# Kernel tuning notes

Hardware: AMD Instinct MI355X
Metric: run time of the kernel (lower is better)

The kernel has to match this reference:

```python
import jax, jax.numpy as jnp
import numpy as np

B, DIN, DH, DOUT = 4096, 512, 1024, 256
DFF = 4 * DH
STEPS = 30
REF_DIM = 64
GAMMA = 0.5 * min(1.0, float(np.sqrt(REF_DIM / DIN)))  # dimension-scaled gamma
LN_EPS = 1e-5


def setup_inputs() -> dict:
    key = jax.random.key(0)
    ks = jax.random.split(key, 6)
    rn = lambda k, shp, s: (jax.random.normal(k, shp, jnp.float32) * s)
    return {
        "x": rn(ks[0], (B, DIN), 1.0),
        "embed_w": rn(ks[1], (DH, DIN), 0.02),
        "embed_b": jnp.zeros((DH,), jnp.float32),
        "W1": rn(ks[2], (DFF, DH), 0.02),
        "b1": jnp.zeros((DFF,), jnp.float32),
        "W2": rn(ks[3], (DH, DFF), 0.02),
        "b2": jnp.zeros((DH,), jnp.float32),
        "ln_g": jnp.ones((DH,), jnp.float32),
        "ln_b": jnp.zeros((DH,), jnp.float32),
        "head_w": rn(ks[4], (DOUT, DH), 0.02),
        "head_b": jnp.zeros((DOUT,), jnp.float32),
    }


def _spectral_normalize(W, n_iter=15):
    # power iteration (u, v treated as constants, like torch spectral_norm buffers)
    v0 = jnp.full((W.shape[1],), 1.0 / np.sqrt(W.shape[1]), W.dtype)
    def body(i, uv):
        _, v = uv
        u = W @ v
        u = u / (jnp.linalg.norm(u) + 1e-12)
        v = W.T @ u
        v = v / (jnp.linalg.norm(v) + 1e-12)
        return (u, v)
    u0 = W @ v0
    u0 = u0 / (jnp.linalg.norm(u0) + 1e-12)
    u, v = jax.lax.fori_loop(0, n_iter, body, (u0, v0))
    u = jax.lax.stop_gradient(u)
    v = jax.lax.stop_gradient(v)
    sigma = u @ (W @ v)  # grad flows through W here, as in torch
    return W / sigma


def _layernorm(h, g, b):
    mu = jnp.mean(h, axis=-1, keepdims=True)
    var = jnp.var(h, axis=-1, keepdims=True)
    return (h - mu) * jax.lax.rsqrt(var + LN_EPS) * g + b


def reference(x, embed_w, embed_b, W1, b1, W2, b2, ln_g, ln_b, head_w, head_b):
    W1n = _spectral_normalize(W1)
    W2n = _spectral_normalize(W2)
    x_emb = x @ embed_w.T + embed_b  # [B, DH]; constant across steps

    def ffn(h):
        hn = _layernorm(h, ln_g, ln_b)
        hid = jnp.tanh(hn @ W1n.T + b1)  # dropout p=0 -> identity
        return hid @ W2n.T + b2

    def step(h, _):
        h_target = ffn(h) + x_emb
        h_next = (1.0 - GAMMA) * h + GAMMA * h_target
        return h_next, None

    h, _ = jax.lax.scan(step, x_emb, None, length=STEPS)
    return h @ head_w.T + head_b
```

## Files before the change

### kernel.cpp

```cpp
#include <hip/hip_runtime.h>
#include <hip/hip_bf16.h>
#include <math.h>

#define B_    4096
#define DIN_  512
#define DH_   1024
#define DOUT_ 256
#define DFF_  4096
#define STEPS_ 30
#define GAMMA_ 0.17677669529663687f
#define LN_EPS_ 1e-5f

typedef __attribute__((ext_vector_type(8))) short short8;
typedef __attribute__((ext_vector_type(4))) float f32x4;

__device__ inline void gload_lds16(const void* g, void* l) {
  __builtin_amdgcn_global_load_lds(
      (const __attribute__((address_space(1))) unsigned int*)g,
      (__attribute__((address_space(3))) unsigned int*)l, 16, 0, 0);
}

__device__ inline float fast_tanh(float v) {
  const float e = __expf(2.f * v);
  return 1.f - 2.f * __builtin_amdgcn_rcpf(e + 1.f);
}

__device__ inline float bf2f(unsigned short u) {
  return __uint_as_float((unsigned)u << 16);
}

__global__ __launch_bounds__(512, 2) void gemm256(
    const __hip_bfloat16* __restrict__ A, const __hip_bfloat16* __restrict__ Bm,
    int M, int N, int K, int kc, int nt, const float* __restrict__ bias,
    int epi, __hip_bfloat16* __restrict__ bf16out) {
  __shared__ __align__(16) char lds[131072];
  const int tid = threadIdx.x;
  const int lane = tid & 63;
  const int wid = tid >> 6;
  const int wr = wid >> 2;
  const int wc = wid & 3;

  const int gx = gridDim.x;
  const int nwg = gx * gridDim.y;
  const int wg = blockIdx.y * gx + blockIdx.x;
  const int cpx = nwg >> 3;
  const int swz = (wg & 7) * cpx + (wg >> 3);
  const int bx = swz % gx, by = swz / gx;
  const int m0 = by * 256, n0 = bx * 256;
  const int zk = blockIdx.z * kc;

  const int scol = ((lane & 7) ^ (lane >> 3)) * 8;
  const int srow = lane >> 3;

  f32x4 acc[8][4];
  const f32x4 zero = {0.f, 0.f, 0.f, 0.f};
#pragma unroll
  for (int i = 0; i < 8; ++i)
#pragma unroll
    for (int j = 0; j < 4; ++j) acc[i][j] = zero;

  auto STAGE = [&](int t) {
    const int kt = zk + t * 64;
    char* ab = &lds[(t & 1) * 32768];
    char* bb = &lds[65536 + (t & 1) * 32768];
#pragma unroll
    for (int i = 0; i < 4; ++i) {
      const int rbase = wid * 32 + i * 8;
      const int r = rbase + srow;
      gload_lds16(A + (size_t)(m0 + r) * K + kt + scol, ab + rbase * 128);
      gload_lds16(Bm + (size_t)(n0 + r) * K + kt + scol, bb + rbase * 128);
    }
  };

  STAGE(0);
  STAGE(1);

  const int ar = lane & 15;
  const int hi = lane >> 4;
  const int a7 = ar & 7;
  const int co0 = ((0 * 4 + hi) ^ a7) * 16;
  const int co1 = ((1 * 4 + hi) ^ a7) * 16;

  for (int t = 0; t < nt; ++t) {
    const int buf = t & 1;
    const char* Ab = &lds[buf * 32768];
    const char* Bb = &lds[65536 + buf * 32768];
    const int arow = (wr * 128 + ar) * 128;
    const int brow = (wc * 64 + ar) * 128;

    if (t == nt - 1) {
      asm volatile("s_waitcnt vmcnt(0)" ::: "memory");
    } else {
      asm volatile("s_waitcnt vmcnt(8)" ::: "memory");
    }
    __builtin_amdgcn_s_barrier();
    __builtin_amdgcn_sched_barrier(0);

    short8 a[4][2], b[4][2];
#pragma unroll
    for (int i = 0; i < 4; ++i) {
      a[i][0] = *(const short8*)(Ab + arow + i * 2048 + co0);
      a[i][1] = *(const short8*)(Ab + arow + i * 2048 + co1);
    }
#pragma unroll
    for (int j = 0; j < 2; ++j) {
      b[j][0] = *(const short8*)(Bb + brow + j * 2048 + co0);
      b[j][1] = *(const short8*)(Bb + brow + j * 2048 + co1);
    }
    asm volatile("s_waitcnt lgkmcnt(0)" ::: "memory");
    __builtin_amdgcn_sched_barrier(0);
    __builtin_amdgcn_s_setprio(1);
#pragma unroll
    for (int i = 0; i < 4; ++i)
#pragma unroll
      for (int j = 0; j < 2; ++j)
#pragma unroll
        for (int ks = 0; ks < 2; ++ks)
          acc[i][j] = __builtin_amdgcn_mfma_f32_16x16x32_bf16(a[i][ks], b[j][ks], acc[i][j], 0, 0, 0);
    __builtin_amdgcn_s_setprio(0);
    __builtin_amdgcn_sched_barrier(0);
#pragma unroll
    for (int j = 0; j < 2; ++j) {
      b[2 + j][0] = *(const short8*)(Bb + brow + (2 + j) * 2048 + co0);
      b[2 + j][1] = *(const short8*)(Bb + brow + (2 + j) * 2048 + co1);
    }
    asm volatile("s_waitcnt lgkmcnt(0)" ::: "memory");
    __builtin_amdgcn_sched_barrier(0);
    __builtin_amdgcn_s_setprio(1);
#pragma unroll
    for (int i = 0; i < 4; ++i)
#pragma unroll
      for (int j = 0; j < 2; ++j)
#pragma unroll
        for (int ks = 0; ks < 2; ++ks)
          acc[i][2 + j] = __builtin_amdgcn_mfma_f32_16x16x32_bf16(a[i][ks], b[2 + j][ks], acc[i][2 + j], 0, 0, 0);
    __builtin_amdgcn_s_setprio(0);
    __builtin_amdgcn_sched_barrier(0);
#pragma unroll
    for (int i = 0; i < 4; ++i) {
      a[i][0] = *(const short8*)(Ab + arow + (4 + i) * 2048 + co0);
      a[i][1] = *(const short8*)(Ab + arow + (4 + i) * 2048 + co1);
    }
    asm volatile("s_waitcnt lgkmcnt(0)" ::: "memory");
    __builtin_amdgcn_sched_barrier(0);
    __builtin_amdgcn_s_setprio(1);
#pragma unroll
    for (int i = 0; i < 4; ++i)
#pragma unroll
      for (int j = 0; j < 2; ++j)
#pragma unroll
        for (int ks = 0; ks < 2; ++ks)
          acc[4 + i][2 + j] = __builtin_amdgcn_mfma_f32_16x16x32_bf16(a[i][ks], b[2 + j][ks], acc[4 + i][2 + j], 0, 0, 0);
    __builtin_amdgcn_s_setprio(0);
    __builtin_amdgcn_sched_barrier(0);
    __builtin_amdgcn_s_setprio(1);
#pragma unroll
    for (int i = 0; i < 4; ++i)
#pragma unroll
      for (int j = 0; j < 2; ++j)
#pragma unroll
        for (int ks = 0; ks < 2; ++ks)
          acc[4 + i][j] = __builtin_amdgcn_mfma_f32_16x16x32_bf16(a[i][ks], b[j][ks], acc[4 + i][j], 0, 0, 0);
    __builtin_amdgcn_s_setprio(0);
    __builtin_amdgcn_sched_barrier(0);
    __builtin_amdgcn_s_barrier();
    __builtin_amdgcn_sched_barrier(0);
    if (t + 2 < nt) STAGE(t + 2);
  }

  if (epi == 4) bf16out += (size_t)blockIdx.z * ((size_t)M * N);
  const int rb = hi * 4;
#pragma unroll
  for (int mf = 0; mf < 8; ++mf) {
#pragma unroll
    for (int nf = 0; nf < 4; ++nf) {
      const int col = n0 + wc * 64 + nf * 16 + ar;
      const float bvs = bias ? bias[col] : 0.f;
#pragma unroll
      for (int j = 0; j < 4; ++j) {
        const int row = m0 + wr * 128 + mf * 16 + rb + j;
        float v = acc[mf][nf][j] + bvs;
        if (epi == 1) v = fast_tanh(v);
        bf16out[(size_t)row * N + col] = __float2bfloat16(v);
      }
    }
  }
}

__global__ __launch_bounds__(256) void gemm_bt(
    const __hip_bfloat16* __restrict__ A, const __hip_bfloat16* __restrict__ Bm,
    int M, int N, int K, const float* __restrict__ bias, int epi,
    float* __restrict__ f32out, float* __restrict__ f32out2) {
  __shared__ __align__(16) short As[128 * 32];
  __shared__ __align__(16) short Bs[128 * 32];
  const int tid = threadIdx.x;
  const int lane = tid & 63;
  const int wid = tid >> 6;
  const int wr = wid >> 1, wc = wid & 1;

  const int gx = gridDim.x;
  const int nwg = gx * gridDim.y;
  const int wg = blockIdx.y * gx + blockIdx.x;
  const int cpx = nwg >> 3;
  const int swz = (wg & 7) * cpx + (wg >> 3);
  const int bx = swz % gx, by = swz / gx;

  const int m0 = by * 128, n0 = bx * 128;
  const int ldsrow = lane >> 2;
  const int col8 = (lane & 3) * 8;

  f32x4 acc[4][4];
  const f32x4 zero = {0.f, 0.f, 0.f, 0.f};
#pragma unroll
  for (int i = 0; i < 4; ++i)
#pragma unroll
    for (int j = 0; j < 4; ++j) acc[i][j] = zero;

  for (int kt = 0; kt < K; kt += 32) {
#pragma unroll
    for (int i = 0; i < 2; ++i) {
      const int seg = wid * 2 + i;
      gload_lds16(A + (size_t)(m0 + seg * 16 + ldsrow) * K + kt + col8,
                  (void*)(As + seg * 512));
      gload_lds16(Bm + (size_t)(n0 + seg * 16 + ldsrow) * K + kt + col8,
                  (void*)(Bs + seg * 512));
    }
    __syncthreads();
    short8 a[4], b[4];
#pragma unroll
    for (int mf = 0; mf < 4; ++mf)
      a[mf] = *(const short8*)&As[(wr * 64 + mf * 16 + (lane & 15)) * 32 + (lane >> 4) * 8];
#pragma unroll
    for (int nf = 0; nf < 4; ++nf)
      b[nf] = *(const short8*)&Bs[(wc * 64 + nf * 16 + (lane & 15)) * 32 + (lane >> 4) * 8];
#pragma unroll
    for (int mf = 0; mf < 4; ++mf)
#pragma unroll
      for (int nf = 0; nf < 4; ++nf)
        acc[mf][nf] = __builtin_amdgcn_mfma_f32_16x16x32_bf16(a[mf], b[nf], acc[mf][nf], 0, 0, 0);
    __syncthreads();
  }

  const int rbase = (lane >> 4) * 4;
  const int cin = lane & 15;
#pragma unroll
  for (int mf = 0; mf < 4; ++mf) {
#pragma unroll
    for (int nf = 0; nf < 4; ++nf) {
      const int col = n0 + wc * 64 + nf * 16 + cin;
      const float bv = bias[col];
#pragma unroll
      for (int j = 0; j < 4; ++j) {
        const int row = m0 + wr * 64 + mf * 16 + rbase + j;
        const float v = acc[mf][nf][j] + bv;
        const size_t idx = (size_t)row * N + col;
        if (epi == 0) {
          f32out[idx] = v;
          f32out2[idx] = v;
        } else {
          f32out[idx] = v;
        }
      }
    }
  }
}

__global__ __launch_bounds__(256) void reduce_ln_kernel(
    const __hip_bfloat16* __restrict__ ps, const float* __restrict__ b2,
    const float* __restrict__ xe, float* __restrict__ h,
    const float* __restrict__ g, const float* __restrict__ be,
    __hip_bfloat16* __restrict__ outbf, int do_ln) {
  const int row = blockIdx.x, tid = threadIdx.x;
  const size_t base = (size_t)row * DH_;
  const size_t slab = (size_t)B_ * DH_;
  float pv0 = 0.f, pv1 = 0.f, pv2 = 0.f, pv3 = 0.f;
#pragma unroll
  for (int z = 0; z < 4; ++z) {
    const ushort4 q = ((const ushort4*)(ps + z * slab + base))[tid];
    pv0 += bf2f(q.x); pv1 += bf2f(q.y); pv2 += bf2f(q.z); pv3 += bf2f(q.w);
  }
  const float4 xv = ((const float4*)(xe + base))[tid];
  const float4 hv = ((const float4*)(h + base))[tid];
  const float4 bv = ((const float4*)b2)[tid];
  float4 nv;
  nv.x = (1.f - GAMMA_) * hv.x + GAMMA_ * (pv0 + bv.x + xv.x);
  nv.y = (1.f - GAMMA_) * hv.y + GAMMA_ * (pv1 + bv.y + xv.y);
  nv.z = (1.f - GAMMA_) * hv.z + GAMMA_ * (pv2 + bv.z + xv.z);
  nv.w = (1.f - GAMMA_) * hv.w + GAMMA_ * (pv3 + bv.w + xv.w);
  ((float4*)(h + base))[tid] = nv;

  __hip_bfloat16* out = outbf + base + tid * 4;
  if (!do_ln) {
    out[0] = __float2bfloat16(nv.x);
    out[1] = __float2bfloat16(nv.y);
    out[2] = __float2bfloat16(nv.z);
    out[3] = __float2bfloat16(nv.w);
    return;
  }
  float s = nv.x + nv.y + nv.z + nv.w;
  float ss = nv.x * nv.x + nv.y * nv.y + nv.z * nv.z + nv.w * nv.w;
#pragma unroll
  for (int o = 32; o > 0; o >>= 1) {
    s += __shfl_down(s, o, 64);
    ss += __shfl_down(ss, o, 64);
  }
  __shared__ float rs_[4], rss_[4];
  const int lane = tid & 63, wid = tid >> 6;
  if (lane == 0) { rs_[wid] = s; rss_[wid] = ss; }
  __syncthreads();
  const float tot = rs_[0] + rs_[1] + rs_[2] + rs_[3];
  const float tots = rss_[0] + rss_[1] + rss_[2] + rss_[3];
  const float mu = tot * (1.f / DH_);
  const float var = tots * (1.f / DH_) - mu * mu;
  const float rstd = rsqrtf(var + LN_EPS_);
  const float4 gv = ((const float4*)g)[tid];
  const float4 bev = ((const float4*)be)[tid];
  out[0] = __float2bfloat16((nv.x - mu) * rstd * gv.x + bev.x);
  out[1] = __float2bfloat16((nv.y - mu) * rstd * gv.y + bev.y);
  out[2] = __float2bfloat16((nv.z - mu) * rstd * gv.z + bev.z);
  out[3] = __float2bfloat16((nv.w - mu) * rstd * gv.w + bev.w);
}

__global__ __launch_bounds__(256) void ln_cast_kernel(
    const float* __restrict__ h, const float* __restrict__ g,
    const float* __restrict__ be, __hip_bfloat16* __restrict__ hn) {
  const int row = blockIdx.x;
  const int tid = threadIdx.x;
  const float4 v = ((const float4*)(h + (size_t)row * DH_))[tid];
  float s = v.x + v.y + v.z + v.w;
  float ss = v.x * v.x + v.y * v.y + v.z * v.z + v.w * v.w;
#pragma unroll
  for (int o = 32; o > 0; o >>= 1) {
    s += __shfl_down(s, o, 64);
    ss += __shfl_down(ss, o, 64);
  }
  __shared__ float rs_[4], rss_[4];
  const int lane = tid & 63, wid = tid >> 6;
  if (lane == 0) { rs_[wid] = s; rss_[wid] = ss; }
  __syncthreads();
  const float tot = rs_[0] + rs_[1] + rs_[2] + rs_[3];
  const float tots = rss_[0] + rss_[1] + rss_[2] + rss_[3];
  const float mu = tot * (1.f / DH_);
  const float var = tots * (1.f / DH_) - mu * mu;
  const float rstd = rsqrtf(var + LN_EPS_);
  const float4 gv = ((const float4*)g)[tid];
  const float4 bv = ((const float4*)be)[tid];
  __hip_bfloat16* out = hn + (size_t)row * DH_ + tid * 4;
  out[0] = __float2bfloat16((v.x - mu) * rstd * gv.x + bv.x);
  out[1] = __float2bfloat16((v.y - mu) * rstd * gv.y + bv.y);
  out[2] = __float2bfloat16((v.z - mu) * rstd * gv.z + bv.z);
  out[3] = __float2bfloat16((v.w - mu) * rstd * gv.w + bv.w);
}

__global__ __launch_bounds__(256) void matvec2_kernel(
    const float* __restrict__ Wa, const float* __restrict__ xa,
    float* __restrict__ ya, int rowsA, int colsA,
    const float* __restrict__ Wb, const float* __restrict__ xb,
    float* __restrict__ yb, int rowsB, int colsB) {
  const int gw = (int)(blockIdx.x * 256 + threadIdx.x) >> 6;
  const int lane = threadIdx.x & 63;
  const float* W;
  const float* x;
  float* y;
  int row, cols;
  if (gw < rowsA) {
    W = Wa; x = xa; y = ya; row = gw; cols = colsA;
  } else {
    row = gw - rowsA;
    if (row >= rowsB) return;
    W = Wb; x = xb; y = yb; cols = colsB;
  }
  const float4* wr = (const float4*)(W + (size_t)row * cols);
  const float4* xv = (const float4*)x;
  const int n4 = cols >> 2;
  float s = 0.f;
  for (int c = lane; c < n4; c += 64) {
    const float4 wv = wr[c];
    const float4 vv = xv[c];
    s += wv.x * vv.x + wv.y * vv.y + wv.z * vv.z + wv.w * vv.w;
  }
#pragma unroll
  for (int o = 32; o > 0; o >>= 1) s += __shfl_down(s, o, 64);
  if (lane == 0) y[row] = s;
}

__global__ __launch_bounds__(256) void transpose_kernel(
    const float* __restrict__ in, float* __restrict__ out, int R, int C) {
  __shared__ float t[32][33];
  const int lx = threadIdx.x & 31, ly = threadIdx.x >> 5;
  const int r0 = blockIdx.y * 32, c0 = blockIdx.x * 32;
#pragma unroll
  for (int j = 0; j < 32; j += 8) t[ly + j][lx] = in[(size_t)(r0 + ly + j) * C + c0 + lx];
  __syncthreads();
#pragma unroll
  for (int j = 0; j < 32; j += 8) out[(size_t)(c0 + ly + j) * R + r0 + lx] = t[lx][ly + j];
}

__global__ void init_v_kernel(float* v1, float* v2) {
  const int i = blockIdx.x * 256 + threadIdx.x;
  if (i < 1024) v1[i] = 0.03125f;
  if (i < 4096) v2[i] = 0.015625f;
}

__global__ __launch_bounds__(256) void cast_kernel(
    const float* __restrict__ s, __hip_bfloat16* __restrict__ d, int n) {
  const int b = (blockIdx.x * 256 + threadIdx.x) * 4;
  if (b < n) {
    const float4 v = *(const float4*)(s + b);
    d[b] = __float2bfloat16(v.x);
    d[b + 1] = __float2bfloat16(v.y);
    d[b + 2] = __float2bfloat16(v.z);
    d[b + 3] = __float2bfloat16(v.w);
  }
}

__global__ __launch_bounds__(256) void cast_scaled_kernel(
    const float* __restrict__ s, __hip_bfloat16* __restrict__ d, int n,
    const float* __restrict__ rs) {
  const float r = rs[0];
  const int b = (blockIdx.x * 256 + threadIdx.x) * 4;
  if (b < n) {
    const float4 v = *(const float4*)(s + b);
    d[b] = __float2bfloat16(v.x * r);
    d[b + 1] = __float2bfloat16(v.y * r);
    d[b + 2] = __float2bfloat16(v.z * r);
    d[b + 3] = __float2bfloat16(v.w * r);
  }
}

__global__ __launch_bounds__(256) void sigma_rs_kernel(
    const float* __restrict__ c, int m, const float* __restrict__ dv, int n,
    float* __restrict__ rs) {
  const int tid = threadIdx.x;
  float sc = 0.f, sd = 0.f;
  for (int i = tid; i < m; i += 256) { const float v = c[i]; sc += v * v; }
  for (int i = tid; i < n; i += 256) { const float v = dv[i]; sd += v * v; }
#pragma unroll
  for (int o = 32; o > 0; o >>= 1) {
    sc += __shfl_down(sc, o, 64);
    sd += __shfl_down(sd, o, 64);
  }
  __shared__ float a[4], b[4];
  const int lane = tid & 63, wid = tid >> 6;
  if (lane == 0) { a[wid] = sc; b[wid] = sd; }
  __syncthreads();
  if (tid == 0) {
    const float tc = a[0] + a[1] + a[2] + a[3];
    const float td = b[0] + b[1] + b[2] + b[3];
    rs[0] = sqrtf(tc / td);
  }
}

extern "C" void kernel_launch(void* const* d_in, const int* in_sizes, int n_in,
                              void* d_out, int out_size, void* d_ws, size_t ws_size,
                              hipStream_t stream) {
  const float* x       = (const float*)d_in[0];
  const float* embed_w = (const float*)d_in[1];
  const float* embed_b = (const float*)d_in[2];
  const float* W1      = (const float*)d_in[3];
  const float* b1      = (const float*)d_in[4];
  const float* W2      = (const float*)d_in[5];
  const float* b2      = (const float*)d_in[6];
  const float* ln_g    = (const float*)d_in[7];
  const float* ln_b    = (const float*)d_in[8];
  const float* head_w  = (const float*)d_in[9];
  const float* head_b  = (const float*)d_in[10];
  float* out = (float*)d_out;

  char* p = (char*)d_ws;
  auto carve = [&](size_t bytes) {
    char* r = p;
    p += (bytes + 255) & ~(size_t)255;
    return (void*)r;
  };
  float* h     = (float*)carve((size_t)B_ * DH_ * 4);
  float* x_emb = (float*)carve((size_t)B_ * DH_ * 4);
  float* W1T   = (float*)carve((size_t)DFF_ * DH_ * 4);
  float* W2T   = (float*)carve((size_t)DH_ * DFF_ * 4);
  __hip_bfloat16* ps = (__hip_bfloat16*)W1T;
  __hip_bfloat16* hn   = (__hip_bfloat16*)carve((size_t)B_ * DH_ * 2);
  __hip_bfloat16* hid  = (__hip_bfloat16*)carve((size_t)B_ * DFF_ * 2);
  __hip_bfloat16* W1n  = (__hip_bfloat16*)carve((size_t)DFF_ * DH_ * 2);
  __hip_bfloat16* W2n  = (__hip_bfloat16*)carve((size_t)DH_ * DFF_ * 2);
  __hip_bfloat16* xbf  = (__hip_bfloat16*)carve((size_t)B_ * DIN_ * 2);
  __hip_bfloat16* ewbf = (__hip_bfloat16*)carve((size_t)DH_ * DIN_ * 2);
  __hip_bfloat16* hwbf = (__hip_bfloat16*)carve((size_t)DOUT_ * DH_ * 2);
  __hip_bfloat16* hbf  = (__hip_bfloat16*)carve((size_t)B_ * DH_ * 2);
  float* v1a = (float*)carve(4096 * 4);
  float* v1b = (float*)carve(4096 * 4);
  float* c1  = (float*)carve(4096 * 4);
  float* v2a = (float*)carve(4096 * 4);
  float* v2b = (float*)carve(4096 * 4);
  float* c2  = (float*)carve(4096 * 4);
  float* rs1 = (float*)carve(256);
  float* rs2 = (float*)carve(256);

  transpose_kernel<<<dim3(DH_ / 32, DFF_ / 32), 256, 0, stream>>>(W1, W1T, DFF_, DH_);
  transpose_kernel<<<dim3(DFF_ / 32, DH_ / 32), 256, 0, stream>>>(W2, W2T, DH_, DFF_);
  init_v_kernel<<<16, 256, 0, stream>>>(v1a, v2a);
  cast_kernel<<<(B_ * DIN_ / 4) / 256, 256, 0, stream>>>(x, xbf, B_ * DIN_);
  cast_kernel<<<(DH_ * DIN_ / 4) / 256, 256, 0, stream>>>(embed_w, ewbf, DH_ * DIN_);
  cast_kernel<<<(DOUT_ * DH_ / 4) / 256, 256, 0, stream>>>(head_w, hwbf, DOUT_ * DH_);

  gemm_bt<<<dim3(DH_ / 128, B_ / 128), 256, 0, stream>>>(
      xbf, ewbf, B_, DH_, DIN_, embed_b, 0, x_emb, h);

  for (int it = 0; it < 15; ++it) {
    const float* vin1 = (it & 1) ? v1b : v1a;
    float* vout1 = (it & 1) ? v1a : v1b;
    const float* vin2 = (it & 1) ? v2b : v2a;
    float* vout2 = (it & 1) ? v2a : v2b;
    matvec2_kernel<<<((DFF_ + DH_) * 64) / 256, 256, 0, stream>>>(
        W1, vin1, c1, DFF_, DH_, W2, vin2, c2, DH_, DFF_);
    matvec2_kernel<<<((DH_ + DFF_) * 64) / 256, 256, 0, stream>>>(
        W1T, c1, vout1, DH_, DFF_, W2T, c2, vout2, DFF_, DH_);
  }
  sigma_rs_kernel<<<1, 256, 0, stream>>>(c1, DFF_, v1b, DH_, rs1);
  sigma_rs_kernel<<<1, 256, 0, stream>>>(c2, DH_, v2b, DFF_, rs2);
  cast_scaled_kernel<<<(DFF_ * DH_ / 4) / 256, 256, 0, stream>>>(W1, W1n, DFF_ * DH_, rs1);
  cast_scaled_kernel<<<(DH_ * DFF_ / 4) / 256, 256, 0, stream>>>(W2, W2n, DH_ * DFF_, rs2);

  ln_cast_kernel<<<B_, 256, 0, stream>>>(h, ln_g, ln_b, hn);

  for (int s = 0; s < STEPS_; ++s) {
    gemm256<<<dim3(DFF_ / 256, B_ / 256, 1), 512, 0, stream>>>(
        hn, W1n, B_, DFF_, DH_, DH_, DH_ / 64, b1, 1, hid);
    gemm256<<<dim3(DH_ / 256, B_ / 256, 4), 512, 0, stream>>>(
        hid, W2n, B_, DH_, DFF_, DFF_ / 4, DFF_ / 4 / 64, nullptr, 4, ps);
    const int last = (s == STEPS_ - 1);
    reduce_ln_kernel<<<B_, 256, 0, stream>>>(
        ps, b2, x_emb, h, ln_g, ln_b, last ? hbf : hn, last ? 0 : 1);
  }

  gemm_bt<<<dim3(DOUT_ / 128, B_ / 128), 256, 0, stream>>>(
      hbf, hwbf, B_, DOUT_, DH_, head_b, 3, out, nullptr);
}
```

Baseline: 3.327 ms.

## Interleave half-tile global-to-LDS loads with MFMA phases in GEMM main loop

Restructures the bf16 GEMM main loop into an 8-phase ping-pong schedule. Each compute phase issues a half-tile global_load_lds for the next K-step and is separated by workgroup barriers, so loads are spread across the iteration rather than issued in one burst after compute. The loop is unrolled by two with fixed LDS buffers, and the waitcnt thresholds are rebalanced. The extra barriers add synchronisation overhead. The unroll assumes the K-tile count is even, and the staging overwrites buffer halves just after they are read, so correctness depends on the barriers holding.

New measurement: 3.268 ms. About the same (-1.8%).

```diff
diff --git a/kernel.cpp b/kernel.cpp
--- a/kernel.cpp
+++ b/kernel.cpp
@@ -59,54 +59,151 @@
 #pragma unroll
     for (int j = 0; j < 4; ++j) acc[i][j] = zero;
 
-  auto STAGE = [&](int t) {
+  auto STG = [&](int t, int hrow, int isB) {
+    if (t >= nt) return;
     const int kt = zk + t * 64;
-    char* ab = &lds[(t & 1) * 32768];
-    char* bb = &lds[65536 + (t & 1) * 32768];
-#pragma unroll
-    for (int i = 0; i < 4; ++i) {
-      const int rbase = wid * 32 + i * 8;
+    char* base = &lds[(t & 1) * 65536 + isB * 32768];
+#pragma unroll
+    for (int j = 0; j < 2; ++j) {
+      const int rbase = hrow + wid * 16 + j * 8;
       const int r = rbase + srow;
-      gload_lds16(A + (size_t)(m0 + r) * K + kt + scol, ab + rbase * 128);
-      gload_lds16(Bm + (size_t)(n0 + r) * K + kt + scol, bb + rbase * 128);
+      const __hip_bfloat16* s =
+          isB ? Bm + (size_t)(n0 + r) * K + kt + scol
+              : A + (size_t)(m0 + r) * K + kt + scol;
+      gload_lds16((const void*)s, (void*)(base + rbase * 128));
     }
   };
 
-  STAGE(0);
-  STAGE(1);
+  STG(0, 0, 1); STG(0, 128, 1); STG(0, 0, 0); STG(0, 128, 0);
+  STG(1, 0, 1); STG(1, 128, 1);
+  asm volatile("s_waitcnt vmcnt(0)" ::: "memory");
+  __builtin_amdgcn_s_barrier();
 
   const int ar = lane & 15;
   const int hi = lane >> 4;
   const int a7 = ar & 7;
-  const int co0 = ((0 * 4 + hi) ^ a7) * 16;
-  const int co1 = ((1 * 4 + hi) ^ a7) * 16;
-
-  for (int t = 0; t < nt; ++t) {
-    const int buf = t & 1;
-    const char* Ab = &lds[buf * 32768];
-    const char* Bb = &lds[65536 + buf * 32768];
-    const int arow = (wr * 128 + ar) * 128;
-    const int brow = (wc * 64 + ar) * 128;
-
-    if (t == nt - 1) {
+  const int co0 = (hi ^ a7) * 16;
+  const int co1 = ((4 + hi) ^ a7) * 16;
+
+  const char* Ab0 = &lds[0];
+  const char* Bb0 = &lds[32768];
+  const char* Ab1 = &lds[65536];
+  const char* Bb1 = &lds[98304];
+  const int arow = (wr * 128 + ar) * 128;
+  const int brow = (wc * 64 + ar) * 128;
+
+  const int niter = nt >> 1;
+  for (int it = 0; it < niter; ++it) {
+    const int t0 = it * 2;
+    const bool lastit = (it == niter - 1);
+    short8 a[4][2], b[4][2];
+
+#pragma unroll
+    for (int i = 0; i < 4; ++i) {
+      a[i][0] = *(const short8*)(Ab0 + arow + i * 2048 + co0);
+      a[i][1] = *(const short8*)(Ab0 + arow + i * 2048 + co1);
+    }
+#pragma unroll
+    for (int j = 0; j < 2; ++j) {
+      b[j][0] = *(const short8*)(Bb0 + brow + j * 2048 + co0);
+      b[j][1] = *(const short8*)(Bb0 + brow + j * 2048 + co1);
+    }
+    STG(t0 + 1, 0, 0);
+    asm volatile("s_waitcnt lgkmcnt(8)" ::: "memory");
+    __builtin_amdgcn_sched_barrier(0);
+    __builtin_amdgcn_s_barrier();
+    asm volatile("s_waitcnt lgkmcnt(0)" ::: "memory");
+    __builtin_amdgcn_sched_barrier(0);
+    __builtin_amdgcn_s_setprio(1);
+#pragma unroll
+    for (int i = 0; i < 4; ++i)
+#pragma unroll
+      for (int j = 0; j < 2; ++j)
+#pragma unroll
+        for (int ks = 0; ks < 2; ++ks)
+          acc[i][j] = __builtin_amdgcn_mfma_f32_16x16x32_bf16(a[i][ks], b[j][ks], acc[i][j], 0, 0, 0);
+    __builtin_amdgcn_s_setprio(0);
+    __builtin_amdgcn_sched_barrier(0);
+    __builtin_amdgcn_s_barrier();
+
+#pragma unroll
+    for (int j = 0; j < 2; ++j) {
+      b[2 + j][0] = *(const short8*)(Bb0 + brow + (2 + j) * 2048 + co0);
+      b[2 + j][1] = *(const short8*)(Bb0 + brow + (2 + j) * 2048 + co1);
+    }
+    STG(t0 + 1, 128, 0);
+    __builtin_amdgcn_sched_barrier(0);
+    __builtin_amdgcn_s_barrier();
+    asm volatile("s_waitcnt lgkmcnt(0)" ::: "memory");
+    __builtin_amdgcn_sched_barrier(0);
+    __builtin_amdgcn_s_setprio(1);
+#pragma unroll
+    for (int i = 0; i < 4; ++i)
+#pragma unroll
+      for (int j = 0; j < 2; ++j)
+#pragma unroll
+        for (int ks = 0; ks < 2; ++ks)
+          acc[i][2 + j] = __builtin_amdgcn_mfma_f32_16x16x32_bf16(a[i][ks], b[2 + j][ks], acc[i][2 + j], 0, 0, 0);
+    __builtin_amdgcn_s_setprio(0);
+    __builtin_amdgcn_sched_barrier(0);
+    __builtin_amdgcn_s_barrier();
+
+#pragma unroll
+    for (int i = 0; i < 4; ++i) {
+      a[i][0] = *(const short8*)(Ab0 + arow + (4 + i) * 2048 + co0);
+      a[i][1] = *(const short8*)(Ab0 + arow + (4 + i) * 2048 + co1);
+    }
+    STG(t0 + 2, 0, 1);
+    __builtin_amdgcn_sched_barrier(0);
+    __builtin_amdgcn_s_barrier();
+    asm volatile("s_waitcnt lgkmcnt(0)" ::: "memory");
+    __builtin_amdgcn_sched_barrier(0);
+    __builtin_amdgcn_s_setprio(1);
+#pragma unroll
+    for (int i = 0; i < 4; ++i)
+#pragma unroll
+      for (int j = 0; j < 2; ++j)
+#pragma unroll
+        for (int ks = 0; ks < 2; ++ks)
+          acc[4 + i][2 + j] = __builtin_amdgcn_mfma_f32_16x16x32_bf16(a[i][ks], b[2 + j][ks], acc[4 + i][2 + j], 0, 0, 0);
+    __builtin_amdgcn_s_setprio(0);
+    __builtin_amdgcn_sched_barrier(0);
+    __builtin_amdgcn_s_barrier();
+
+    STG(t0 + 2, 128, 1);
+    if (lastit) {
       asm volatile("s_waitcnt vmcnt(0)" ::: "memory");
     } else {
-      asm volatile("s_waitcnt vmcnt(8)" ::: "memory");
-    }
-    __builtin_amdgcn_s_barrier();
-    __builtin_amdgcn_sched_barrier(0);
-
-    short8 a[4][2], b[4][2];
+      asm volatile("s_waitcnt vmcnt(4)" ::: "memory");
+    }
+    __builtin_amdgcn_sched_barrier(0);
+    __builtin_amdgcn_s_barrier();
+    __builtin_amdgcn_s_setprio(1);
+#pragma unroll
+    for (int i = 0; i < 4; ++i)
+#pragma unroll
+      for (int j = 0; j < 2; ++j)
+#pragma unroll
+        for (int ks = 0; ks < 2; ++ks)
+          acc[4 + i][j] = __builtin_amdgcn_mfma_f32_16x16x32_bf16(a[i][ks], b[j][ks], acc[4 + i][j], 0, 0, 0);
+    __builtin_amdgcn_s_setprio(0);
+    __builtin_amdgcn_sched_barrier(0);
+    __builtin_amdgcn_s_barrier();
+
 #pragma unroll
     for (int i = 0; i < 4; ++i) {
-      a[i][0] = *(const short8*)(Ab + arow + i * 2048 + co0);
-      a[i][1] = *(const short8*)(Ab + arow + i * 2048 + co1);
+      a[i][0] = *(const short8*)(Ab1 + arow + i * 2048 + co0);
+      a[i][1] = *(const short8*)(Ab1 + arow + i * 2048 + co1);
     }
 #pragma unroll
     for (int j = 0; j < 2; ++j) {
-      b[j][0] = *(const short8*)(Bb + brow + j * 2048 + co0);
-      b[j][1] = *(const short8*)(Bb + brow + j * 2048 + co1);
-    }
+      b[j][0] = *(const short8*)(Bb1 + brow + j * 2048 + co0);
+      b[j][1] = *(const short8*)(Bb1 + brow + j * 2048 + co1);
+    }
+    STG(t0 + 2, 0, 0);
+    asm volatile("s_waitcnt lgkmcnt(8)" ::: "memory");
+    __builtin_amdgcn_sched_barrier(0);
+    __builtin_amdgcn_s_barrier();
     asm volatile("s_waitcnt lgkmcnt(0)" ::: "memory");
     __builtin_amdgcn_sched_barrier(0);
     __builtin_amdgcn_s_setprio(1);
@@ -119,11 +216,16 @@
           acc[i][j] = __builtin_amdgcn_mfma_f32_16x16x32_bf16(a[i][ks], b[j][ks], acc[i][j], 0, 0, 0);
     __builtin_amdgcn_s_setprio(0);
     __builtin_amdgcn_sched_barrier(0);
+    __builtin_amdgcn_s_barrier();
+
 #pragma unroll
     for (int j = 0; j < 2; ++j) {
-      b[2 + j][0] = *(const short8*)(Bb + brow + (2 + j) * 2048 + co0);
-      b[2 + j][1] = *(const short8*)(Bb + brow + (2 + j) * 2048 + co1);
-    }
+      b[2 + j][0] = *(const short8*)(Bb1 + brow + (2 + j) * 2048 + co0);
+      b[2 + j][1] = *(const short8*)(Bb1 + brow + (2 + j) * 2048 + co1);
+    }
+    STG(t0 + 2, 128, 0);
+    __builtin_amdgcn_sched_barrier(0);
+    __builtin_amdgcn_s_barrier();
     asm volatile("s_waitcnt lgkmcnt(0)" ::: "memory");
     __builtin_amdgcn_sched_barrier(0);
     __builtin_amdgcn_s_setprio(1);
@@ -136,11 +238,16 @@
           acc[i][2 + j] = __builtin_amdgcn_mfma_f32_16x16x32_bf16(a[i][ks], b[2 + j][ks], acc[i][2 + j], 0, 0, 0);
     __builtin_amdgcn_s_setprio(0);
     __builtin_amdgcn_sched_barrier(0);
+    __builtin_amdgcn_s_barrier();
+
 #pragma unroll
     for (int i = 0; i < 4; ++i) {
-      a[i][0] = *(const short8*)(Ab + arow + (4 + i) * 2048 + co0);
-      a[i][1] = *(const short8*)(Ab + arow + (4 + i) * 2048 + co1);
-    }
+      a[i][0] = *(const short8*)(Ab1 + arow + (4 + i) * 2048 + co0);
+      a[i][1] = *(const short8*)(Ab1 + arow + (4 + i) * 2048 + co1);
+    }
+    STG(t0 + 3, 0, 1);
+    __builtin_amdgcn_sched_barrier(0);
+    __builtin_amdgcn_s_barrier();
     asm volatile("s_waitcnt lgkmcnt(0)" ::: "memory");
     __builtin_amdgcn_sched_barrier(0);
     __builtin_amdgcn_s_setprio(1);
@@ -153,6 +260,12 @@
           acc[4 + i][2 + j] = __builtin_amdgcn_mfma_f32_16x16x32_bf16(a[i][ks], b[2 + j][ks], acc[4 + i][2 + j], 0, 0, 0);
     __builtin_amdgcn_s_setprio(0);
     __builtin_amdgcn_sched_barrier(0);
+    __builtin_amdgcn_s_barrier();
+
+    STG(t0 + 3, 128, 1);
+    asm volatile("s_waitcnt vmcnt(4)" ::: "memory");
+    __builtin_amdgcn_sched_barrier(0);
+    __builtin_amdgcn_s_barrier();
     __builtin_amdgcn_s_setprio(1);
 #pragma unroll
     for (int i = 0; i < 4; ++i)
@@ -164,8 +277,6 @@
     __builtin_amdgcn_s_setprio(0);
     __builtin_amdgcn_sched_barrier(0);
     __builtin_amdgcn_s_barrier();
-    __builtin_amdgcn_sched_barrier(0);
-    if (t + 2 < nt) STAGE(t + 2);
   }
 
   if (epi == 4) bf16out += (size_t)blockIdx.z * ((size_t)M * N);
```
